# Performance work log

Hardware: AMD Instinct MI355X
Metric: run time of the kernel (lower is better)

The kernel has to match this reference:

```python
import jax, jax.numpy as jnp
import numpy as np

NUM_HEADS = 16
NEG_BIG = -1.0e9


def setup_inputs() -> dict:
    key = jax.random.key(0)
    k1, k2, k3 = jax.random.split(key, 3)
    B, S, D = 2, 2048, 1024
    x = jax.random.normal(k1, (B, S, D), dtype=jnp.float32)
    qkv_weights = jax.random.normal(k2, (D, 3 * D), dtype=jnp.float32) * (1.0 / np.sqrt(D))
    output_weights = jax.random.normal(k3, (D, D), dtype=jnp.float32) * (1.0 / np.sqrt(D))
    return {"x": x, "qkv_weights": qkv_weights, "output_weights": output_weights}


def reference(x, qkv_weights, output_weights):
    B, S, D = x.shape
    H = NUM_HEADS
    hd = D // H
    qkv = jnp.einsum('bsd,de->bse', x, qkv_weights)  # [B,S,3D]
    q, k, v = jnp.split(qkv, 3, axis=-1)
    # [B,H,S,hd]
    q = q.reshape(B, S, H, hd).transpose(0, 2, 1, 3)
    k = k.reshape(B, S, H, hd).transpose(0, 2, 1, 3)
    v = v.reshape(B, S, H, hd).transpose(0, 2, 1, 3)
    scores = jnp.einsum('bhqd,bhkd->bhqk', q, k)  # unscaled, matches original masked path
    # original bug: when masked, softmax is applied to UNSCALED scores with mask
    tril = jnp.tril(jnp.ones((S, S), dtype=scores.dtype))
    masked = scores * tril + NEG_BIG * (1.0 - tril)
    attn = jax.nn.softmax(masked, axis=-1)
    heads = jnp.einsum('bhqk,bhkd->bhqd', attn, v)  # [B,H,S,hd]
    merged = heads.transpose(0, 2, 1, 3).reshape(B, S, D)
    return jnp.einsum('bsd,de->bse', merged, output_weights)
```

## Files before the change

kernel.cpp:

```cpp
#include <hip/hip_runtime.h>
#include <stdint.h>

using u16 = unsigned short;
typedef __attribute__((ext_vector_type(8))) _Float16 half8;
typedef __attribute__((ext_vector_type(4))) float f32x4;
typedef __attribute__((ext_vector_type(4))) unsigned short u16x4;
typedef __attribute__((ext_vector_type(8))) unsigned short u16x8;

#define S_LEN 2048
#define D_MODEL 1024
#define NHEAD 16
#define HDIM 64

__device__ __forceinline__ u16 f2h_bits(float f){
    _Float16 h = (_Float16)f;
    return __builtin_bit_cast(u16, h);
}
__device__ __forceinline__ float h2f_bits(u16 v){
    return (float)__builtin_bit_cast(_Float16, v);
}

typedef __attribute__((address_space(1))) void gvoid;
typedef __attribute__((address_space(3))) void lvoid;
__device__ __forceinline__ void gload_lds16(const u16* g, u16* l){
    __builtin_amdgcn_global_load_lds((gvoid*)(uintptr_t)g, (lvoid*)l, 16, 0, 0);
}

__global__ __launch_bounds__(256) void k_cvt_w(const float* __restrict__ W0, u16* __restrict__ T0,
                                               const float* __restrict__ W1, u16* __restrict__ T1){
    __shared__ float tt[32][33];
    int bx = blockIdx.x;
    const float* W; u16* WT; int N, n0;
    if (bx < 96){ W = W0; WT = T0; N = 3072; n0 = bx*32; }
    else        { W = W1; WT = T1; N = 1024; n0 = (bx-96)*32; }
    int k0 = blockIdx.y*32;
    int tx = threadIdx.x & 31, ty = threadIdx.x >> 5;
    #pragma unroll
    for (int i=0;i<4;++i) tt[ty+8*i][tx] = W[(size_t)(k0+ty+8*i)*N + n0+tx];
    __syncthreads();
    #pragma unroll
    for (int i=0;i<4;++i) WT[(size_t)(n0+ty+8*i)*1024 + k0+tx] = f2h_bits(tt[tx][ty+8*i]);
}

template<int EPI>
__global__ __launch_bounds__(256) void k_gemm(const void* __restrict__ Ap, const u16* __restrict__ BT,
                                              float* __restrict__ Cf, u16* __restrict__ Qh,
                                              u16* __restrict__ Kh, u16* __restrict__ Vt){
    constexpr int Kd = 1024;
    __shared__ u16 As[2*128*32];
    __shared__ u16 Bs[2*128*32];
    int nwg = gridDim.x;
    int cpx = nwg >> 3;
    int wg  = ((int)blockIdx.x & 7)*cpx + ((int)blockIdx.x >> 3);
    int tm = wg & 31, tn = wg >> 5;
    int t = threadIdx.x;
    int w = t >> 6, lane = t & 63;
    int lr = lane & 15, lg = lane >> 4;
    int wm = (w>>1)*64, wn = (w&1)*64;
    int m0 = tm*128 + wm, n0 = tn*128 + wn;

    const u16* bG = BT + (size_t)(tn*128 + (t>>2))*Kd + (t&3)*8;
    u16* bL = Bs + (t>>2)*32 + (t&3)*8;
    auto stageB = [&](int buf, int kk){
        gload_lds16(bG + kk, bL + buf*4096);
        gload_lds16(bG + kk + (size_t)64*Kd, bL + buf*4096 + 64*32);
    };

    const float* aF = nullptr; u16* aW = nullptr;
    const u16*  aG = nullptr; u16* aL = nullptr;
    if constexpr (EPI==1){
        aF = (const float*)Ap + (size_t)(tm*128 + (t>>1))*Kd + (t&1)*16;
        aW = As + (t>>1)*32 + (t&1)*16;
    } else {
        aG = (const u16*)Ap + (size_t)(tm*128 + (t>>2))*Kd + (t&3)*8;
        aL = As + (t>>2)*32 + (t&3)*8;
    }
    float4 fa0, fa1, fa2, fa3;
    auto loadA = [&](int kk){
        fa0 = *reinterpret_cast<const float4*>(aF + kk);
        fa1 = *reinterpret_cast<const float4*>(aF + kk + 4);
        fa2 = *reinterpret_cast<const float4*>(aF + kk + 8);
        fa3 = *reinterpret_cast<const float4*>(aF + kk + 12);
    };
    auto writeA = [&](int buf){
        u16x8 p0, p1;
        p0[0]=f2h_bits(fa0.x); p0[1]=f2h_bits(fa0.y); p0[2]=f2h_bits(fa0.z); p0[3]=f2h_bits(fa0.w);
        p0[4]=f2h_bits(fa1.x); p0[5]=f2h_bits(fa1.y); p0[6]=f2h_bits(fa1.z); p0[7]=f2h_bits(fa1.w);
        p1[0]=f2h_bits(fa2.x); p1[1]=f2h_bits(fa2.y); p1[2]=f2h_bits(fa2.z); p1[3]=f2h_bits(fa2.w);
        p1[4]=f2h_bits(fa3.x); p1[5]=f2h_bits(fa3.y); p1[6]=f2h_bits(fa3.z); p1[7]=f2h_bits(fa3.w);
        *reinterpret_cast<u16x8*>(aW + buf*4096)     = p0;
        *reinterpret_cast<u16x8*>(aW + buf*4096 + 8) = p1;
    };
    auto stageA0 = [&](int buf, int kk){
        gload_lds16(aG + kk, aL + buf*4096);
        gload_lds16(aG + kk + (size_t)64*Kd, aL + buf*4096 + 64*32);
    };

    f32x4 acc[4][4];
    #pragma unroll
    for (int i=0;i<4;++i)
        #pragma unroll
        for (int j=0;j<4;++j) acc[i][j] = (f32x4){0.f,0.f,0.f,0.f};

    if constexpr (EPI==1){ loadA(0); stageB(0,0); writeA(0); }
    else                 { stageA0(0,0); stageB(0,0); }
    __syncthreads();

    for (int kk=0; kk<Kd; kk+=32){
        int cur = (kk>>5) & 1;
        bool more = (kk+32 < Kd);
        if (more){
            if constexpr (EPI==1) loadA(kk+32);
            else                  stageA0(cur^1, kk+32);
            stageB(cur^1, kk+32);
        }

        half8 av[4], bv[4];
        #pragma unroll
        for (int mf=0;mf<4;++mf) av[mf] = *reinterpret_cast<const half8*>(&As[cur*4096 + (wm+mf*16+lr)*32 + lg*8]);
        #pragma unroll
        for (int nf=0;nf<4;++nf) bv[nf] = *reinterpret_cast<const half8*>(&Bs[cur*4096 + (wn+nf*16+lr)*32 + lg*8]);
        __builtin_amdgcn_s_setprio(1);
        #pragma unroll
        for (int mf=0;mf<4;++mf)
            #pragma unroll
            for (int nf=0;nf<4;++nf)
                acc[mf][nf] = __builtin_amdgcn_mfma_f32_16x16x32_f16(av[mf], bv[nf], acc[mf][nf], 0,0,0);
        __builtin_amdgcn_s_setprio(0);
        if (more){
            if constexpr (EPI==1) writeA(cur^1);
        }
        __syncthreads();
    }

    if (EPI == 0){
        #pragma unroll
        for (int mf=0;mf<4;++mf)
            #pragma unroll
            for (int nf=0;nf<4;++nf)
                #pragma unroll
                for (int j=0;j<4;++j)
                    Cf[(size_t)(m0+mf*16+lg*4+j)*D_MODEL + n0+nf*16+lr] = acc[mf][nf][j];
    } else {
        #pragma unroll
        for (int mf=0;mf<4;++mf){
            int r0 = m0 + mf*16 + lg*4;
            int b  = r0 >> 11, s = r0 & 2047;
            #pragma unroll
            for (int nf=0;nf<4;++nf){
                int col = n0 + nf*16 + lr;
                int which = col >> 10;
                int d  = col & 1023;
                int h  = d >> 6, di = d & 63;
                int bh = b*NHEAD + h;
                if (which == 2){
                    u16x4 pv;
                    pv.x = f2h_bits(acc[mf][nf][0]);
                    pv.y = f2h_bits(acc[mf][nf][1]);
                    pv.z = f2h_bits(acc[mf][nf][2]);
                    pv.w = f2h_bits(acc[mf][nf][3]);
                    *reinterpret_cast<u16x4*>(Vt + ((size_t)bh*HDIM + di)*S_LEN + s) = pv;
                } else {
                    u16* dst = (which==0 ? Qh : Kh) + ((size_t)bh*S_LEN + s)*HDIM + di;
                    #pragma unroll
                    for (int j=0;j<4;++j) dst[(size_t)j*HDIM] = f2h_bits(acc[mf][nf][j]);
                }
            }
        }
    }
}

__global__ __launch_bounds__(256,3) void k_attn(const u16* __restrict__ Q, const u16* __restrict__ K,
                                                const u16* __restrict__ Vt, u16* __restrict__ Mg,
                                                u16* __restrict__ On, float* __restrict__ Ml,
                                                float* __restrict__ Ll){
    __shared__ u16 Kl[2*64*64];
    __shared__ u16 Vl[2*64*64];
    __shared__ u16 plds[4][32][72];
    int t = threadIdx.x;
    int w = t >> 6, lane = t & 63;
    int lr = lane & 15, lg = lane >> 4;
    int blk = blockIdx.x;
    int bh  = blk & 31;
    int p   = blk >> 5;
    int qb, ktLo, ktHi, part; bool split;
    if (p < 8)      { qb = p;    ktLo = 0;      ktHi = 2*p+2;   split = false; part = 0; }
    else if (p < 16){ qb = 23-p; ktLo = 0;      ktHi = qb+1;    split = true;  part = 0; }
    else            { qb = 31-p; ktLo = qb+1;   ktHi = 2*qb+2;  split = true;  part = 1; }
    int q0w = qb*128 + w*32;
    int b = bh >> 4, h = bh & 15;
    int pid = split ? ((bh<<3) + (qb-8))*2 + part : 0;
    const u16* Qp = Q  + (size_t)bh*S_LEN*HDIM;
    const u16* Kp = K  + (size_t)bh*S_LEN*HDIM;
    const u16* Vp = Vt + (size_t)bh*HDIM*S_LEN;

    int c0 = t, c1 = t + 256;
    int r0 = c0 >> 3, s0 = 8*((c0 & 7) ^ (r0 & 7));
    int r1 = c1 >> 3, s1 = 8*((c1 & 7) ^ (r1 & 7));
    const u16* Ks0 = Kp + (size_t)r0*HDIM + s0;
    const u16* Ks1 = Kp + (size_t)r1*HDIM + s1;
    const u16* Vs0 = Vp + (size_t)r0*S_LEN + s0;
    const u16* Vs1 = Vp + (size_t)r1*S_LEN + s1;
    u16* Kd0 = Kl + c0*8; u16* Kd1 = Kl + c1*8;
    u16* Vd0 = Vl + c0*8; u16* Vd1 = Vl + c1*8;

    auto stageKV = [&](int buf, int kt){
        int kbase = kt*64;
        gload_lds16(Ks0 + (size_t)kbase*HDIM, Kd0 + buf*4096);
        gload_lds16(Ks1 + (size_t)kbase*HDIM, Kd1 + buf*4096);
        gload_lds16(Vs0 + kbase, Vd0 + buf*4096);
        gload_lds16(Vs1 + kbase, Vd1 + buf*4096);
    };

    half8 qf[2][2];
    #pragma unroll
    for (int qi=0;qi<2;++qi)
        #pragma unroll
        for (int ks=0;ks<2;++ks){
            half8 v = *reinterpret_cast<const half8*>(Qp + (size_t)(q0w+qi*16+lr)*HDIM + ks*32 + lg*8);
            #pragma unroll
            for (int j=0;j<8;++j) v[j] = v[j] * (_Float16)1.44269504f;
            qf[qi][ks] = v;
        }

    f32x4 oacc[2][4];
    float mrow[2], lrow[2];
    #pragma unroll
    for (int mf=0;mf<2;++mf){
        #pragma unroll
        for (int nf=0;nf<4;++nf) oacc[mf][nf] = (f32x4){0.f,0.f,0.f,0.f};
        mrow[mf] = -1e30f; lrow[mf] = 0.f;
    }

    int lastkt = (q0w + 31) >> 6;
    int swz = (lr & 7)*8;
    int nT = ktHi - ktLo;

    stageKV(0, ktLo);
    __syncthreads();
    for (int i=0; i<nT; ++i){
        int kt = ktLo + i;
        int cur = i & 1;
        if (i+1 < nT) stageKV(cur^1, kt+1);

        if (kt <= lastkt){
            const u16* Kb = Kl + cur*4096;
            const u16* Vb = Vl + cur*4096;
            int kbase = kt*64;
            half8 kfr[4][2];
            #pragma unroll
            for (int kf=0;kf<4;++kf)
                #pragma unroll
                for (int ks=0;ks<2;++ks)
                    kfr[kf][ks] = *reinterpret_cast<const half8*>(Kb + (kf*16+lr)*64 + ((ks*32 + lg*8) ^ swz));
            f32x4 sc[4][2];
            #pragma unroll
            for (int kf=0;kf<4;++kf)
                #pragma unroll
                for (int qi=0;qi<2;++qi) sc[kf][qi] = (f32x4){0.f,0.f,0.f,0.f};
            __builtin_amdgcn_s_setprio(1);
            #pragma unroll
            for (int kf=0;kf<4;++kf)
                #pragma unroll
                for (int qi=0;qi<2;++qi)
                    #pragma unroll
                    for (int ks=0;ks<2;++ks)
                        sc[kf][qi] = __builtin_amdgcn_mfma_f32_16x16x32_f16(kfr[kf][ks], qf[qi][ks], sc[kf][qi], 0,0,0);
            __builtin_amdgcn_s_setprio(0);

            half8 vf[4][2];
            #pragma unroll
            for (int nf=0;nf<4;++nf)
                #pragma unroll
                for (int kh=0;kh<2;++kh)
                    vf[nf][kh] = *reinterpret_cast<const half8*>(Vb + (nf*16+lr)*64 + ((kh*32 + lg*8) ^ swz));

            if (kt == lastkt){
                #pragma unroll
                for (int kf=0;kf<4;++kf)
                    #pragma unroll
                    for (int qi=0;qi<2;++qi)
                        #pragma unroll
                        for (int j=0;j<4;++j)
                            if (kbase+kf*16+lg*4+j > q0w+qi*16+lr) sc[kf][qi][j] = -1e9f;
            }

            float pmax[2];
            #pragma unroll
            for (int qi=0;qi<2;++qi){
                float t0 = fmaxf(fmaxf(sc[0][qi][0], sc[0][qi][1]), fmaxf(sc[0][qi][2], sc[0][qi][3]));
                float t1 = fmaxf(fmaxf(sc[1][qi][0], sc[1][qi][1]), fmaxf(sc[1][qi][2], sc[1][qi][3]));
                float t2 = fmaxf(fmaxf(sc[2][qi][0], sc[2][qi][1]), fmaxf(sc[2][qi][2], sc[2][qi][3]));
                float t3 = fmaxf(fmaxf(sc[3][qi][0], sc[3][qi][1]), fmaxf(sc[3][qi][2], sc[3][qi][3]));
                float tm = fmaxf(fmaxf(t0,t1), fmaxf(t2,t3));
                tm = fmaxf(tm, __shfl_xor(tm,16));
                tm = fmaxf(tm, __shfl_xor(tm,32));
                pmax[qi] = tm;
            }
            bool need = (pmax[0] > mrow[0]+8.0f) || (pmax[1] > mrow[1]+8.0f);
            if (__any(need)){
                float aq[2];
                #pragma unroll
                for (int qi=0;qi<2;++qi){
                    float mnew = fmaxf(mrow[qi], pmax[qi]);
                    aq[qi] = __builtin_amdgcn_exp2f(mrow[qi] - mnew);
                    mrow[qi] = mnew;
                    lrow[qi] *= aq[qi];
                }
                float am[2][4];
                #pragma unroll
                for (int mf=0;mf<2;++mf)
                    #pragma unroll
                    for (int j=0;j<4;++j) am[mf][j] = __shfl(aq[mf], lg*4+j);
                #pragma unroll
                for (int mf=0;mf<2;++mf)
                    #pragma unroll
                    for (int nf=0;nf<4;++nf)
                        #pragma unroll
                        for (int j=0;j<4;++j) oacc[mf][nf][j] *= am[mf][j];
            }
            #pragma unroll
            for (int qi=0;qi<2;++qi){
                float m = mrow[qi];
                float rs = 0.f;
                #pragma unroll
                for (int kf=0;kf<4;++kf)
                    #pragma unroll
                    for (int j=0;j<4;++j){
                        float e = __builtin_amdgcn_exp2f(sc[kf][qi][j] - m);
                        sc[kf][qi][j] = e;
                        rs += e;
                    }
                rs += __shfl_xor(rs,16);
                rs += __shfl_xor(rs,32);
                lrow[qi] += rs;
            }
            #pragma unroll
            for (int kf=0;kf<4;++kf)
                #pragma unroll
                for (int qi=0;qi<2;++qi){
                    u16x4 pk;
                    pk.x = f2h_bits(sc[kf][qi][0]);
                    pk.y = f2h_bits(sc[kf][qi][1]);
                    pk.z = f2h_bits(sc[kf][qi][2]);
                    pk.w = f2h_bits(sc[kf][qi][3]);
                    *reinterpret_cast<u16x4*>(&plds[w][qi*16+lr][kf*16+lg*4]) = pk;
                }
            half8 pa[2][2];
            #pragma unroll
            for (int mf=0;mf<2;++mf)
                #pragma unroll
                for (int kh=0;kh<2;++kh)
                    pa[mf][kh] = *reinterpret_cast<const half8*>(&plds[w][mf*16+lr][kh*32 + lg*8]);
            __builtin_amdgcn_s_setprio(1);
            #pragma unroll
            for (int mf=0;mf<2;++mf)
                #pragma unroll
                for (int nf=0;nf<4;++nf)
                    #pragma unroll
                    for (int kh=0;kh<2;++kh)
                        oacc[mf][nf] = __builtin_amdgcn_mfma_f32_16x16x32_f16(pa[mf][kh], vf[nf][kh], oacc[mf][nf], 0,0,0);
            __builtin_amdgcn_s_setprio(0);
        }
        __syncthreads();
    }

    float linv[2][4];
    #pragma unroll
    for (int mf=0;mf<2;++mf)
        #pragma unroll
        for (int j=0;j<4;++j) linv[mf][j] = 1.0f/__shfl(lrow[mf], lg*4+j);
    if (!split){
        #pragma unroll
        for (int mf=0;mf<2;++mf)
            #pragma unroll
            for (int nf=0;nf<4;++nf)
                #pragma unroll
                for (int j=0;j<4;++j)
                    Mg[(size_t)(b*S_LEN + q0w + mf*16 + lg*4 + j)*D_MODEL + h*HDIM + nf*16 + lr]
                        = f2h_bits(oacc[mf][nf][j]*linv[mf][j]);
    } else {
        #pragma unroll
        for (int mf=0;mf<2;++mf)
            #pragma unroll
            for (int nf=0;nf<4;++nf)
                #pragma unroll
                for (int j=0;j<4;++j)
                    On[pid*8192 + (w*32 + mf*16 + lg*4 + j)*64 + nf*16 + lr]
                        = f2h_bits(oacc[mf][nf][j]*linv[mf][j]);
        if (lg == 0){
            #pragma unroll
            for (int qi=0;qi<2;++qi){
                Ml[pid*128 + w*32 + qi*16 + lr] = mrow[qi];
                Ll[pid*128 + w*32 + qi*16 + lr] = lrow[qi];
            }
        }
    }
}

__global__ __launch_bounds__(256) void k_comb(const u16* __restrict__ On, const float* __restrict__ Ml,
                                              const float* __restrict__ Ll, u16* __restrict__ Mg){
    int blk = blockIdx.x;
    int bh = blk & 31;
    int q8 = blk >> 5;
    int qb = 8 + q8;
    int b = bh >> 4, h = bh & 15;
    int t = threadIdx.x;
    int c = t & 63, rg = t >> 6;
    int pid0 = ((bh<<3) + q8)*2, pid1 = pid0 + 1;
    #pragma unroll 4
    for (int i=0;i<32;++i){
        int r = rg*32 + i;
        float m1 = Ml[pid0*128 + r], m2 = Ml[pid1*128 + r];
        float l1 = Ll[pid0*128 + r], l2 = Ll[pid1*128 + r];
        float M  = fmaxf(m1, m2);
        float w1 = l1*__builtin_amdgcn_exp2f(m1 - M);
        float w2 = l2*__builtin_amdgcn_exp2f(m2 - M);
        float o1 = h2f_bits(On[pid0*8192 + r*64 + c]);
        float o2 = h2f_bits(On[pid1*8192 + r*64 + c]);
        float o  = (w1*o1 + w2*o2) / (w1 + w2);
        Mg[(size_t)(b*S_LEN + qb*128 + r)*D_MODEL + h*HDIM + c] = f2h_bits(o);
    }
}

extern "C" void kernel_launch(void* const* d_in, const int* in_sizes, int n_in,
                              void* d_out, int out_size, void* d_ws, size_t ws_size,
                              hipStream_t stream) {
    const float* x    = (const float*)d_in[0];
    const float* wqkv = (const float*)d_in[1];
    const float* wout = (const float*)d_in[2];
    float* out = (float*)d_out;
    char* ws = (char*)d_ws;

    const size_t MB = 1u<<20;
    u16* wqkvT  = (u16*)(ws + 8*MB);
    u16* woutT  = (u16*)(ws + 14*MB);
    u16* Qh     = (u16*)(ws + 16*MB);
    u16* Kh     = (u16*)(ws + 24*MB);
    u16* Vt     = (u16*)(ws + 32*MB);
    u16* Mg     = (u16*)(ws + 40*MB);
    u16* On     = (u16*)(ws + 48*MB);
    float* Ml   = (float*)(ws + 56*MB);
    float* Ll   = (float*)(ws + 56*MB + 256*1024);

    k_cvt_w <<<dim3(128,32), 256, 0, stream>>>(wqkv, wqkvT, wout, woutT);
    k_gemm<1><<<768, 256, 0, stream>>>((const void*)x, wqkvT, nullptr, Qh, Kh, Vt);
    k_attn  <<<768, 256, 0, stream>>>(Qh, Kh, Vt, Mg, On, Ml, Ll);
    k_comb  <<<256, 256, 0, stream>>>(On, Ml, Ll, Mg);
    k_gemm<0><<<256, 256, 0, stream>>>((const void*)Mg, woutT, out, nullptr, nullptr, nullptr);
}
```

Baseline: 121.3 us.

## Prefetch A two stages ahead and XOR-swizzle A tile in LDS

The fp32 A-operand global loads in the GEMM are now issued two K-steps ahead using two register buffers, and the main loop is unrolled by two with fixed LDS buffer indices. The A tile written to LDS also uses an XOR swizzle on its 8-element chunks, with matching read addressing, to cut bank conflicts on the fp16 stores and fragment reads. The aim is to hide more global-load latency behind MFMA work and to lower LDS conflict stalls, at the cost of extra registers for the second buffer. The loop assumes Kd is a multiple of 64, and the final writeA stores unused data into a buffer after the last MFMA step.

After: 139.8 us. 1.15x slower.

```diff
diff --git a/kernel.cpp b/kernel.cpp
--- a/kernel.cpp
+++ b/kernel.cpp
@@ -66,30 +66,32 @@
         gload_lds16(bG + kk + (size_t)64*Kd, bL + buf*4096 + 64*32);
     };
 
-    const float* aF = nullptr; u16* aW = nullptr;
+    const float* aF = nullptr; u16 *aW0 = nullptr, *aW1 = nullptr;
     const u16*  aG = nullptr; u16* aL = nullptr;
     if constexpr (EPI==1){
-        aF = (const float*)Ap + (size_t)(tm*128 + (t>>1))*Kd + (t&1)*16;
-        aW = As + (t>>1)*32 + (t&1)*16;
+        int rA = t>>1, cA = t&1, sw = (rA>>1)&3;
+        aF  = (const float*)Ap + (size_t)(tm*128 + rA)*Kd + cA*16;
+        aW0 = As + rA*32 + (((2*cA  ) ^ sw)*8);
+        aW1 = As + rA*32 + (((2*cA+1) ^ sw)*8);
     } else {
         aG = (const u16*)Ap + (size_t)(tm*128 + (t>>2))*Kd + (t&3)*8;
         aL = As + (t>>2)*32 + (t&3)*8;
     }
-    float4 fa0, fa1, fa2, fa3;
-    auto loadA = [&](int kk){
-        fa0 = *reinterpret_cast<const float4*>(aF + kk);
-        fa1 = *reinterpret_cast<const float4*>(aF + kk + 4);
-        fa2 = *reinterpret_cast<const float4*>(aF + kk + 8);
-        fa3 = *reinterpret_cast<const float4*>(aF + kk + 12);
-    };
-    auto writeA = [&](int buf){
+    float4 fa[4], fb[4];
+    auto loadA = [&](float4* d, int kk){
+        d[0] = *reinterpret_cast<const float4*>(aF + kk);
+        d[1] = *reinterpret_cast<const float4*>(aF + kk + 4);
+        d[2] = *reinterpret_cast<const float4*>(aF + kk + 8);
+        d[3] = *reinterpret_cast<const float4*>(aF + kk + 12);
+    };
+    auto writeA = [&](int buf, const float4* s){
         u16x8 p0, p1;
-        p0[0]=f2h_bits(fa0.x); p0[1]=f2h_bits(fa0.y); p0[2]=f2h_bits(fa0.z); p0[3]=f2h_bits(fa0.w);
-        p0[4]=f2h_bits(fa1.x); p0[5]=f2h_bits(fa1.y); p0[6]=f2h_bits(fa1.z); p0[7]=f2h_bits(fa1.w);
-        p1[0]=f2h_bits(fa2.x); p1[1]=f2h_bits(fa2.y); p1[2]=f2h_bits(fa2.z); p1[3]=f2h_bits(fa2.w);
-        p1[4]=f2h_bits(fa3.x); p1[5]=f2h_bits(fa3.y); p1[6]=f2h_bits(fa3.z); p1[7]=f2h_bits(fa3.w);
-        *reinterpret_cast<u16x8*>(aW + buf*4096)     = p0;
-        *reinterpret_cast<u16x8*>(aW + buf*4096 + 8) = p1;
+        p0[0]=f2h_bits(s[0].x); p0[1]=f2h_bits(s[0].y); p0[2]=f2h_bits(s[0].z); p0[3]=f2h_bits(s[0].w);
+        p0[4]=f2h_bits(s[1].x); p0[5]=f2h_bits(s[1].y); p0[6]=f2h_bits(s[1].z); p0[7]=f2h_bits(s[1].w);
+        p1[0]=f2h_bits(s[2].x); p1[1]=f2h_bits(s[2].y); p1[2]=f2h_bits(s[2].z); p1[3]=f2h_bits(s[2].w);
+        p1[4]=f2h_bits(s[3].x); p1[5]=f2h_bits(s[3].y); p1[6]=f2h_bits(s[3].z); p1[7]=f2h_bits(s[3].w);
+        *reinterpret_cast<u16x8*>(aW0 + buf*4096) = p0;
+        *reinterpret_cast<u16x8*>(aW1 + buf*4096) = p1;
     };
     auto stageA0 = [&](int buf, int kk){
         gload_lds16(aG + kk, aL + buf*4096);
@@ -102,22 +104,12 @@
         #pragma unroll
         for (int j=0;j<4;++j) acc[i][j] = (f32x4){0.f,0.f,0.f,0.f};
 
-    if constexpr (EPI==1){ loadA(0); stageB(0,0); writeA(0); }
-    else                 { stageA0(0,0); stageB(0,0); }
-    __syncthreads();
-
-    for (int kk=0; kk<Kd; kk+=32){
-        int cur = (kk>>5) & 1;
-        bool more = (kk+32 < Kd);
-        if (more){
-            if constexpr (EPI==1) loadA(kk+32);
-            else                  stageA0(cur^1, kk+32);
-            stageB(cur^1, kk+32);
-        }
-
+    int chA = (EPI==1) ? (lg ^ ((lr>>1)&3)) : lg;
+
+    auto mfmaStep = [&](int cur){
         half8 av[4], bv[4];
         #pragma unroll
-        for (int mf=0;mf<4;++mf) av[mf] = *reinterpret_cast<const half8*>(&As[cur*4096 + (wm+mf*16+lr)*32 + lg*8]);
+        for (int mf=0;mf<4;++mf) av[mf] = *reinterpret_cast<const half8*>(&As[cur*4096 + (wm+mf*16+lr)*32 + chA*8]);
         #pragma unroll
         for (int nf=0;nf<4;++nf) bv[nf] = *reinterpret_cast<const half8*>(&Bs[cur*4096 + (wn+nf*16+lr)*32 + lg*8]);
         __builtin_amdgcn_s_setprio(1);
@@ -127,9 +119,30 @@
             for (int nf=0;nf<4;++nf)
                 acc[mf][nf] = __builtin_amdgcn_mfma_f32_16x16x32_f16(av[mf], bv[nf], acc[mf][nf], 0,0,0);
         __builtin_amdgcn_s_setprio(0);
-        if (more){
-            if constexpr (EPI==1) writeA(cur^1);
-        }
+    };
+
+    if constexpr (EPI==1){
+        loadA(fa, 0); stageB(0, 0);
+        writeA(0, fa);
+        loadA(fb, 32);
+    } else {
+        stageA0(0, 0); stageB(0, 0);
+    }
+    __syncthreads();
+
+    for (int kk=0; kk<Kd; kk+=64){
+        if constexpr (EPI==1){ if (kk+64 < Kd) loadA(fa, kk+64); }
+        else                 { stageA0(1, kk+32); }
+        stageB(1, kk+32);
+        mfmaStep(0);
+        if constexpr (EPI==1) writeA(1, fb);
+        __syncthreads();
+
+        if constexpr (EPI==1){ if (kk+96 < Kd) loadA(fb, kk+96); }
+        else                 { if (kk+64 < Kd) stageA0(0, kk+64); }
+        if (kk+64 < Kd) stageB(0, kk+64);
+        mfmaStep(1);
+        if constexpr (EPI==1) writeA(0, fa);
         __syncthreads();
     }
 
```

## Rebalance causal attention work with table-driven multi-way KV splits

Applied to the files above, without the earlier changes.

Replaces the fixed scheme (8 unsplit query blocks plus 8 blocks split in two) with constant lookup tables. These split the longer query blocks into 2–4 key-range chunks of roughly equal size, so the grid grows from 768 to 1280 workgroups. The combine kernel is generalised to merge a variable number of partials per query block, and the workspace layout is shifted to fit the larger partial buffers. The goal is better load balance and less tail imbalance across CUs, at the cost of more partial-output traffic and a heavier combine step.

New measurement: 179.2 us. +47.7%, slower.

```diff
diff --git a/kernel.cpp b/kernel.cpp
--- a/kernel.cpp
+++ b/kernel.cpp
@@ -25,6 +25,13 @@
 __device__ __forceinline__ void gload_lds16(const u16* g, u16* l){
     __builtin_amdgcn_global_load_lds((gvoid*)(uintptr_t)g, (lvoid*)l, 16, 0, 0);
 }
+
+__device__ __constant__ signed char QB_T[40] = {3,7,7,10,11,11,11,14,14,15,15,15,15, 6,6,9,9,10,10,12,12,13,13,13,13,14,14, 2,5,5,8,8,8,9,12,12, 4,4, 1, 0};
+__device__ __constant__ signed char LO_T[40] = {0,0,8,0,0,8,16,0,8,0,8,16,24, 0,7,0,7,8,15,0,7,0,7,14,21,16,23, 0,0,6,0,6,12,14,14,20, 0,5, 0, 0};
+__device__ __constant__ signed char HI_T[40] = {8,8,16,8,8,16,24,8,16,8,16,24,32, 7,14,7,14,15,22,7,14,7,14,21,28,23,30, 6,6,12,6,12,18,20,20,26, 5,10, 4, 2};
+__device__ __constant__ signed char PO_T[40] = {-1,6,7,14,17,18,19,28,29,32,33,34,35, 4,5,11,12,15,16,20,21,24,25,26,27,30,31, -1,2,3,8,9,10,13,22,23, 0,1, -1, -1};
+__device__ __constant__ signed char NP_T[12] = {2,2,2,2,3,3,3,3,4,4,4,4};
+__device__ __constant__ signed char OF_T[12] = {0,2,4,6,8,11,14,17,20,24,28,32};
 
 __global__ __launch_bounds__(256) void k_cvt_w(const float* __restrict__ W0, u16* __restrict__ T0,
                                                const float* __restrict__ W1, u16* __restrict__ T1){
@@ -182,14 +189,15 @@
     int lr = lane & 15, lg = lane >> 4;
     int blk = blockIdx.x;
     int bh  = blk & 31;
-    int p   = blk >> 5;
-    int qb, ktLo, ktHi, part; bool split;
-    if (p < 8)      { qb = p;    ktLo = 0;      ktHi = 2*p+2;   split = false; part = 0; }
-    else if (p < 16){ qb = 23-p; ktLo = 0;      ktHi = qb+1;    split = true;  part = 0; }
-    else            { qb = 31-p; ktLo = qb+1;   ktHi = 2*qb+2;  split = true;  part = 1; }
+    int pi  = blk >> 5;
+    int qb   = QB_T[pi];
+    int ktLo = LO_T[pi];
+    int ktHi = HI_T[pi];
+    int po   = PO_T[pi];
+    bool split = (po >= 0);
     int q0w = qb*128 + w*32;
     int b = bh >> 4, h = bh & 15;
-    int pid = split ? ((bh<<3) + (qb-8))*2 + part : 0;
+    int pid = split ? bh*36 + po : 0;
     const u16* Qp = Q  + (size_t)bh*S_LEN*HDIM;
     const u16* Kp = K  + (size_t)bh*S_LEN*HDIM;
     const u16* Vp = Vt + (size_t)bh*HDIM*S_LEN;
@@ -386,7 +394,7 @@
             for (int nf=0;nf<4;++nf)
                 #pragma unroll
                 for (int j=0;j<4;++j)
-                    On[pid*8192 + (w*32 + mf*16 + lg*4 + j)*64 + nf*16 + lr]
+                    On[(size_t)pid*8192 + (w*32 + mf*16 + lg*4 + j)*64 + nf*16 + lr]
                         = f2h_bits(oacc[mf][nf][j]*linv[mf][j]);
         if (lg == 0){
             #pragma unroll
@@ -402,24 +410,36 @@
                                               const float* __restrict__ Ll, u16* __restrict__ Mg){
     int blk = blockIdx.x;
     int bh = blk & 31;
-    int q8 = blk >> 5;
-    int qb = 8 + q8;
+    int qi = blk >> 5;
+    int qb = 4 + qi;
+    int np = NP_T[qi];
+    int base = bh*36 + OF_T[qi];
     int b = bh >> 4, h = bh & 15;
     int t = threadIdx.x;
     int c = t & 63, rg = t >> 6;
-    int pid0 = ((bh<<3) + q8)*2, pid1 = pid0 + 1;
     #pragma unroll 4
     for (int i=0;i<32;++i){
         int r = rg*32 + i;
-        float m1 = Ml[pid0*128 + r], m2 = Ml[pid1*128 + r];
-        float l1 = Ll[pid0*128 + r], l2 = Ll[pid1*128 + r];
-        float M  = fmaxf(m1, m2);
-        float w1 = l1*__builtin_amdgcn_exp2f(m1 - M);
-        float w2 = l2*__builtin_amdgcn_exp2f(m2 - M);
-        float o1 = h2f_bits(On[pid0*8192 + r*64 + c]);
-        float o2 = h2f_bits(On[pid1*8192 + r*64 + c]);
-        float o  = (w1*o1 + w2*o2) / (w1 + w2);
-        Mg[(size_t)(b*S_LEN + qb*128 + r)*D_MODEL + h*HDIM + c] = f2h_bits(o);
+        float mm[4], ll[4];
+        float M = -1e30f;
+        #pragma unroll
+        for (int p=0;p<4;++p){
+            if (p < np){
+                mm[p] = Ml[(base+p)*128 + r];
+                ll[p] = Ll[(base+p)*128 + r];
+                M = fmaxf(M, mm[p]);
+            }
+        }
+        float osum = 0.f, wsum = 0.f;
+        #pragma unroll
+        for (int p=0;p<4;++p){
+            if (p < np){
+                float wgt = ll[p]*__builtin_amdgcn_exp2f(mm[p] - M);
+                osum += wgt*h2f_bits(On[(size_t)(base+p)*8192 + r*64 + c]);
+                wsum += wgt;
+            }
+        }
+        Mg[(size_t)(b*S_LEN + qb*128 + r)*D_MODEL + h*HDIM + c] = f2h_bits(osum/wsum);
     }
 }
 
@@ -433,19 +453,19 @@
     char* ws = (char*)d_ws;
 
     const size_t MB = 1u<<20;
-    u16* wqkvT  = (u16*)(ws + 8*MB);
-    u16* woutT  = (u16*)(ws + 14*MB);
-    u16* Qh     = (u16*)(ws + 16*MB);
-    u16* Kh     = (u16*)(ws + 24*MB);
-    u16* Vt     = (u16*)(ws + 32*MB);
-    u16* Mg     = (u16*)(ws + 40*MB);
-    u16* On     = (u16*)(ws + 48*MB);
-    float* Ml   = (float*)(ws + 56*MB);
-    float* Ll   = (float*)(ws + 56*MB + 256*1024);
+    u16* wqkvT  = (u16*)(ws + 0*MB);
+    u16* woutT  = (u16*)(ws + 6*MB);
+    u16* Qh     = (u16*)(ws + 8*MB);
+    u16* Kh     = (u16*)(ws + 16*MB);
+    u16* Vt     = (u16*)(ws + 24*MB);
+    u16* Mg     = (u16*)(ws + 32*MB);
+    u16* On     = (u16*)(ws + 40*MB);
+    float* Ml   = (float*)(ws + 59*MB);
+    float* Ll   = (float*)(ws + 59*MB + 640*1024);
 
     k_cvt_w <<<dim3(128,32), 256, 0, stream>>>(wqkv, wqkvT, wout, woutT);
     k_gemm<1><<<768, 256, 0, stream>>>((const void*)x, wqkvT, nullptr, Qh, Kh, Vt);
-    k_attn  <<<768, 256, 0, stream>>>(Qh, Kh, Vt, Mg, On, Ml, Ll);
-    k_comb  <<<256, 256, 0, stream>>>(On, Ml, Ll, Mg);
+    k_attn  <<<1280, 256, 0, stream>>>(Qh, Kh, Vt, Mg, On, Ml, Ll);
+    k_comb  <<<384, 256, 0, stream>>>(On, Ml, Ll, Mg);
     k_gemm<0><<<256, 256, 0, stream>>>((const void*)Mg, woutT, out, nullptr, nullptr, nullptr);
 }
```
